# Performance work log

Measured on AMD Instinct MI355X. Metric: run time of the kernel, lower is better.

Reference implementation:

```python
import jax, jax.numpy as jnp
import numpy as np

B, S, H, NH = 2, 2048, 2048, 16
HD = H // NH  # head_dim = 128


def setup_inputs() -> dict:
    key = jax.random.key(0)
    ks = jax.random.split(key, 6)
    scale = 1.0 / np.sqrt(H)
    hidden_state = jax.random.normal(ks[0], (B, S, H), dtype=jnp.float32)
    # upper-triangular (strictly above diagonal) = 1 -> masked positions
    causal_mask = jnp.triu(jnp.ones((S, S), dtype=jnp.float32), k=1)[None, None]
    Wq = jax.random.normal(ks[1], (H, H), dtype=jnp.float32) * scale
    Wk = jax.random.normal(ks[2], (H, H), dtype=jnp.float32) * scale
    Wv = jax.random.normal(ks[3], (H, H), dtype=jnp.float32) * scale
    Wo = jax.random.normal(ks[4], (H, H), dtype=jnp.float32) * scale
    zeros = jnp.zeros((H,), dtype=jnp.float32)
    return {"hidden_state": hidden_state, "causal_mask": causal_mask,
            "Wq": Wq, "bq": zeros, "Wk": Wk, "bk": zeros,
            "Wv": Wv, "bv": zeros, "Wo": Wo, "bo": zeros}


def reference(hidden_state, causal_mask, Wq, bq, Wk, bk, Wv, bv, Wo, bo):
    b, s, h = hidden_state.shape
    q = (hidden_state @ Wq.T + bq).reshape(b, s, NH, HD).transpose(0, 2, 1, 3)  # [B,NH,S,HD]
    k = (hidden_state @ Wk.T + bk).reshape(b, s, NH, HD).transpose(0, 2, 1, 3)
    v = (hidden_state @ Wv.T + bv).reshape(b, s, NH, HD).transpose(0, 2, 1, 3)
    scores = jnp.einsum('bhqd,bhkd->bhqk', q, k) / jnp.sqrt(jnp.float32(HD))
    scores = scores + causal_mask * (-1e9)
    probs = jax.nn.softmax(scores, axis=-1)
    out = jnp.einsum('bhqk,bhkd->bhqd', probs, v)
    out = out.transpose(0, 2, 1, 3).reshape(b, s, h)
    return out @ Wo.T + bo
```

## Files before the change

kernel.cpp:

```cpp
#include <hip/hip_runtime.h>
#include <hip/hip_bf16.h>
#include <stdint.h>

#define B_   2
#define S_   2048
#define H_   2048
#define NH_  16
#define HD_  128
#define MTOT (B_*S_)

typedef __attribute__((ext_vector_type(8))) short bf16x8;
typedef __attribute__((ext_vector_type(4))) short bf16x4;
typedef __attribute__((ext_vector_type(4))) float f32x4;

__device__ __forceinline__ void gload_lds16(const void* g, void* l) {
    __builtin_amdgcn_global_load_lds(
        (const __attribute__((address_space(1))) void*)g,
        (__attribute__((address_space(3))) void*)l, 16, 0, 0);
}

__device__ __forceinline__ unsigned short f2bfu(float x) {
    __hip_bfloat16 h = __float2bfloat16(x);
    return *reinterpret_cast<unsigned short*>(&h);
}
__device__ __forceinline__ int packbf(float a, float b) {
    return (int)f2bfu(a) | ((int)f2bfu(b) << 16);
}

#define BAR()  asm volatile("s_barrier" ::: "memory")
#define WLG0() asm volatile("s_waitcnt lgkmcnt(0)" ::: "memory")
#define WVM(n) asm volatile("s_waitcnt vmcnt(" #n ")" ::: "memory")

__global__ void castall(const float* __restrict__ hs,
                        const float* __restrict__ w0, const float* __restrict__ w1,
                        const float* __restrict__ w2, const float* __restrict__ w3,
                        __hip_bfloat16* __restrict__ xb,
                        __hip_bfloat16* __restrict__ o0, __hip_bfloat16* __restrict__ o1,
                        __hip_bfloat16* __restrict__ o2, __hip_bfloat16* __restrict__ o3)
{
    const size_t Q = 1048576;
    const float* in; __hip_bfloat16* out; size_t base = 0;
    switch (blockIdx.y) {
        case 0:  in = hs; out = xb; break;
        case 1:  in = hs; out = xb; base = Q; break;
        case 2:  in = w0; out = o0; break;
        case 3:  in = w1; out = o1; break;
        case 4:  in = w2; out = o2; break;
        default: in = w3; out = o3; break;
    }
    size_t i = base + (size_t)blockIdx.x * 256 + threadIdx.x;
    float4 v = *(const float4*)(in + i * 4);
    uint2 o;
    o.x = (unsigned)packbf(v.x, v.y);
    o.y = (unsigned)packbf(v.z, v.w);
    *(uint2*)((char*)out + i * 8) = o;
}

template<int SMEMB, int BF16OUT>
__device__ __forceinline__ void gemm_body(const __hip_bfloat16* __restrict__ Ablk,
                                          const __hip_bfloat16* __restrict__ Wblk,
                                          const float* __restrict__ bias,
                                          void* __restrict__ Cout,
                                          int N, int K, int br, int bc)
{
    __shared__ __align__(16) char smem[SMEMB];
    __hip_bfloat16* As = (__hip_bfloat16*)smem;
    __hip_bfloat16* Bs = (__hip_bfloat16*)(smem + 8192);

    const int tid  = threadIdx.x;
    const int wave = tid >> 6, lane = tid & 63;
    const int quad = lane >> 4, l16 = lane & 15;
    const int wr = wave >> 1, wc = wave & 1;

    f32x4 acc[4][4] = {};

    for (int k0 = 0; k0 < K; k0 += 32) {
#pragma unroll
        for (int t = 0; t < 2; ++t) {
            int c = t * 256 + wave * 64 + lane;
            int row = c >> 2, cc = c & 3;
            int base = (t * 256 + wave * 64) * 16;
            gload_lds16(Ablk + (size_t)row * K + k0 + cc * 8, (char*)As + base);
            gload_lds16(Wblk + (size_t)row * K + k0 + cc * 8, (char*)Bs + base);
        }
        __syncthreads();

        bf16x8 af[4], bf[4];
#pragma unroll
        for (int i = 0; i < 4; ++i)
            af[i] = *(const bf16x8*)&As[(wr * 64 + i * 16 + l16) * 32 + quad * 8];
#pragma unroll
        for (int j = 0; j < 4; ++j)
            bf[j] = *(const bf16x8*)&Bs[(wc * 64 + j * 16 + l16) * 32 + quad * 8];

#pragma unroll
        for (int i = 0; i < 4; ++i)
#pragma unroll
            for (int j = 0; j < 4; ++j)
                acc[i][j] = __builtin_amdgcn_mfma_f32_16x16x32_bf16(af[i], bf[j], acc[i][j], 0, 0, 0);
        __syncthreads();
    }

#pragma unroll
    for (int i = 0; i < 4; ++i) {
        int row = br * 128 + wr * 64 + i * 16 + quad * 4;
#pragma unroll
        for (int j = 0; j < 4; ++j) {
            int col = bc * 128 + wc * 64 + j * 16 + l16;
            float bv = bias[col];
#pragma unroll
            for (int r = 0; r < 4; ++r) {
                float v = acc[i][j][r] + bv;
                if (BF16OUT)
                    ((__hip_bfloat16*)Cout)[(size_t)(row + r) * N + col] = __float2bfloat16(v);
                else
                    ((float*)Cout)[(size_t)(row + r) * N + col] = v;
            }
        }
    }
}

__global__ __launch_bounds__(256)
void gemm_out(const __hip_bfloat16* __restrict__ A, const __hip_bfloat16* __restrict__ W,
              const float* __restrict__ bias, float* __restrict__ C)
{
    gemm_body<16384, 0>(A + (size_t)(blockIdx.y * 128) * H_, W + (size_t)(blockIdx.x * 128) * H_,
                        bias, C, H_, H_, blockIdx.y, blockIdx.x);
}

template<int EPI>
__device__ __forceinline__ void gemm256x128_body(const __hip_bfloat16* __restrict__ Xp,
                                                 const __hip_bfloat16* __restrict__ Wp,
                                                 const float* __restrict__ bias,
                                                 void* __restrict__ Cout,
                                                 int bm, int bn, char* smem)
{
    const int tid  = threadIdx.x;
    const int wave = tid >> 6, lane = tid & 63;
    const int quad = lane >> 4, l16 = lane & 15;
    const int wr = wave >> 2, wc = wave & 3;

    const int ro = l16 * 64;
    const int co = (((l16 & 8) ? ((quad * 8) ^ 16) : (quad * 8)) << 1);

    int r0, c0, r1, c1;
    {
        int D = tid * 16;
        int rg = D >> 11, cg = (D >> 10) & 1;
        int rr = (D >> 6) & 15, c = (D & 63) >> 1;
        int cs = (rr & 8) ? (c ^ 16) : c;
        r0 = rg * 16 + rr;  c0 = cg * 32 + cs;
        D = 8192 + tid * 16;
        rg = D >> 11; cg = (D >> 10) & 1;
        rr = (D >> 6) & 15; c = (D & 63) >> 1;
        cs = (rr & 8) ? (c ^ 16) : c;
        r1 = rg * 16 + rr;  c1 = cg * 32 + cs;
    }

    char* const A0h = smem + wr * 16384;
    char* const A1h = smem + 32768 + wr * 16384;
    char* const B0h = smem + 65536 + (wc >> 1) * 8192;
    char* const B1h = smem + 81920 + (wc >> 1) * 8192;
    const int bsub = (wc & 1) * 2;

    auto STG = [&](char* ldsb, const __hip_bfloat16* g) {
        gload_lds16(g + (size_t)r0 * H_ + c0, ldsb + wave * 1024);
        gload_lds16(g + (size_t)r1 * H_ + c1, ldsb + 8192 + wave * 1024);
    };
    auto STG1 = [&](char* ldsb, const __hip_bfloat16* g) {
        gload_lds16(g + (size_t)r0 * H_ + c0, ldsb + wave * 1024);
    };
    auto SRCA = [&](const __hip_bfloat16* P, int t, int hf) {
        return P + (size_t)(hf * 128) * H_ + (size_t)t * 64;
    };
    auto SRCB = [&](const __hip_bfloat16* P, int t, int hf) {
        return P + (size_t)(hf * 64) * H_ + (size_t)t * 64;
    };

    f32x4 acc[8][2] = {};

    STG (smem,          SRCA(Xp, 0, 0));
    STG (smem + 16384,  SRCA(Xp, 0, 1));
    STG1(smem + 65536,        SRCB(Wp, 0, 0));
    STG1(smem + 65536 + 8192, SRCB(Wp, 0, 1));
    STG1(smem + 81920,        SRCB(Wp, 1, 0));
    STG1(smem + 81920 + 8192, SRCB(Wp, 1, 1));
    WVM(2);
    BAR();

    const int NIT = H_ / 128;
    bf16x8 bfr[2][2];
    for (int j = 0; j < NIT; ++j) {
        const bool more = (j < NIT - 1);
        const int t1 = 2 * j + 1;
#pragma unroll
        for (int ph = 0; ph < 8; ++ph) {
            const int p = ph & 3;
            char* aA = (ph < 4) ? A0h : A1h;
            char* aB = (ph < 4) ? B0h : B1h;

            if (p == 0) {
#pragma unroll
                for (int jj = 0; jj < 2; ++jj)
#pragma unroll
                    for (int kk = 0; kk < 2; ++kk)
                        bfr[jj][kk] = *(const bf16x8*)(aB + ((bsub + jj) * 2 + kk) * 1024 + ro + co);
            }
            bf16x8 af[2][2];
#pragma unroll
            for (int i2 = 0; i2 < 2; ++i2)
#pragma unroll
                for (int kk = 0; kk < 2; ++kk)
                    af[i2][kk] = *(const bf16x8*)(aA + ((2 * p + i2) * 2 + kk) * 1024 + ro + co);

            if (ph == 0) { STG(smem + 32768, SRCA(Xp, t1, 0));
                           STG(smem + 49152, SRCA(Xp, t1, 1)); }
            else if (ph == 1 && more) STG1(smem + 65536,        SRCB(Wp, t1 + 1, 0));
            else if (ph == 2 && more) STG1(smem + 65536 + 8192, SRCB(Wp, t1 + 1, 1));
            else if (ph == 4 && more) STG (smem,                SRCA(Xp, t1 + 1, 0));
            else if (ph == 5 && more) STG (smem + 16384,        SRCA(Xp, t1 + 1, 1));
            else if (ph == 6 && more) STG1(smem + 81920,        SRCB(Wp, t1 + 2, 0));
            else if (ph == 7 && more) STG1(smem + 81920 + 8192, SRCB(Wp, t1 + 2, 1));

            if (ph == 3) { if (more) { WVM(2); } else { WVM(0); } }
            if (ph == 7 && more) { WVM(2); }

            BAR();
            WLG0();
            __builtin_amdgcn_sched_barrier(0);
            __builtin_amdgcn_s_setprio(1);
#pragma unroll
            for (int kk = 0; kk < 2; ++kk)
#pragma unroll
                for (int i2 = 0; i2 < 2; ++i2)
#pragma unroll
                    for (int jj = 0; jj < 2; ++jj)
                        acc[2 * p + i2][jj] = __builtin_amdgcn_mfma_f32_16x16x32_bf16(
                            af[i2][kk], bfr[jj][kk], acc[2 * p + i2][jj], 0, 0, 0);
            __builtin_amdgcn_s_setprio(0);
            BAR();
        }
    }

    if (EPI == 2) {
        __hip_bfloat16* VTo = (__hip_bfloat16*)Cout;
#pragma unroll
        for (int i = 0; i < 8; ++i) {
            int tok = bm * 256 + wr * 128 + i * 16 + quad * 4;
            int b = tok >> 11, s = tok & (S_ - 1);
#pragma unroll
            for (int jj = 0; jj < 2; ++jj) {
                int col = bn * 128 + (wc >> 1) * 64 + (wc & 1) * 32 + jj * 16 + l16;
                int h = col >> 7, d = col & 127;
                float bv = bias[col];
                bf16x4 v;
#pragma unroll
                for (int r = 0; r < 4; ++r)
                    v[r] = (short)f2bfu(acc[i][jj][r] + bv);
                *(bf16x4*)(VTo + ((size_t)(b * 16 + h) * 128 + d) * S_ + s) = v;
            }
        }
    } else {
#pragma unroll
        for (int i = 0; i < 8; ++i) {
            int row = bm * 256 + wr * 128 + i * 16 + quad * 4;
#pragma unroll
            for (int jj = 0; jj < 2; ++jj) {
                int col = bn * 128 + (wc >> 1) * 64 + (wc & 1) * 32 + jj * 16 + l16;
                float bv = bias[col];
#pragma unroll
                for (int r = 0; r < 4; ++r)
                    ((__hip_bfloat16*)Cout)[(size_t)(row + r) * H_ + col] =
                        __float2bfloat16(acc[i][jj][r] + bv);
            }
        }
    }
}

__global__ __launch_bounds__(512, 2)
void gemm_qkv8(const __hip_bfloat16* __restrict__ X,
               const __hip_bfloat16* __restrict__ Wq, const __hip_bfloat16* __restrict__ Wk,
               const __hip_bfloat16* __restrict__ Wv,
               const float* __restrict__ bq, const float* __restrict__ bk,
               const float* __restrict__ bv,
               __hip_bfloat16* __restrict__ Qo, __hip_bfloat16* __restrict__ Ko,
               __hip_bfloat16* __restrict__ VTo)
{
    __shared__ __align__(16) char smem[98304];

    const int bid = blockIdx.x;
    const int swz = (bid & 7) * 96 + (bid >> 3);
    const int sel = swz >> 8;
    const int rem = swz & 255;
    const int bn  = rem & 15;
    const int bm  = rem >> 4;

    const __hip_bfloat16* W = (sel == 0) ? Wq : (sel == 1) ? Wk : Wv;
    const float* bias       = (sel == 0) ? bq : (sel == 1) ? bk : bv;

    const __hip_bfloat16* Xp = X + (size_t)(bm * 256) * H_;
    const __hip_bfloat16* Wp = W + (size_t)(bn * 128) * H_;

    if (sel == 2)
        gemm256x128_body<2>(Xp, Wp, bias, VTo, bm, bn, smem);
    else
        gemm256x128_body<1>(Xp, Wp, bias, (sel == 0) ? Qo : Ko, bm, bn, smem);
}

__global__ __launch_bounds__(256)
void attn_kernel(const __hip_bfloat16* __restrict__ Q,
                 const __hip_bfloat16* __restrict__ K,
                 const __hip_bfloat16* __restrict__ VT,
                 __hip_bfloat16* __restrict__ O)
{
    __shared__ __align__(16) char Ks[2][16384];
    __shared__ __align__(16) char Vt[2][16384];

    const int tid  = threadIdx.x;
    const int wave = tid >> 6, lane = tid & 63;
    const int quad = lane >> 4, l16 = lane & 15;

    const int lid = blockIdx.x;
    const int xcd = lid & 7;
    const int q   = lid >> 3;
    const int bh  = ((q >> 5) << 3) | xcd;
    const int qb  = 31 - (q & 31);
    const int b   = bh >> 4, h = bh & 15;

    const size_t headoff = (size_t)b * S_ * H_ + (size_t)h * HD_;
    const __hip_bfloat16* Qp  = Q + headoff;
    const __hip_bfloat16* Kp  = K + headoff;
    const __hip_bfloat16* Vtp = VT + (size_t)(b * 16 + h) * 128 * S_;

    const float scale  = 0.08838834764831843f;
    const float THRraw = 90.50966799187809f;
    const int A0 = (((quad & 1) * 2) * 16 + l16) * 4;
    const int A1 = A0 + 64;
    const bool hiq = (quad >= 2);

    const int qrow_local = wave * 16;
    const int qrow = qb * 64 + qrow_local;

    bf16x8 qf[4];
#pragma unroll
    for (int kd = 0; kd < 4; ++kd)
        qf[kd] = *(const bf16x8*)(Qp + (size_t)(qrow + l16) * H_ + kd * 32 + quad * 8);

    f32x4 oacc[8] = {};
    float mi = -1e30f, li = 0.0f;

#pragma unroll
    for (int t = 0; t < 4; ++t) {
        int c = wave * 256 + t * 64 + lane;
        int krow = c >> 4, kpos = c & 15;
        gload_lds16(Kp + (size_t)krow * H_ + (kpos ^ (krow & 7)) * 8,
                    &Ks[0][(wave * 256 + t * 64) * 16]);
        int vrow = c >> 3, vpos = c & 7;
        gload_lds16(Vtp + (size_t)vrow * S_ + (vpos ^ (vrow & 7)) * 8,
                    &Vt[0][(wave * 256 + t * 64) * 16]);
    }
    __syncthreads();

    for (int kb = 0; kb <= qb; ++kb) {
        const int cur = kb & 1;
        const bool more = (kb < qb);

        if (more) {
            const __hip_bfloat16* Kn = Kp + (size_t)(kb + 1) * 64 * H_;
            const int vcol = (kb + 1) * 64;
#pragma unroll
            for (int t = 0; t < 4; ++t) {
                int c = wave * 256 + t * 64 + lane;
                int krow = c >> 4, kpos = c & 15;
                gload_lds16(Kn + (size_t)krow * H_ + (kpos ^ (krow & 7)) * 8,
                            &Ks[cur ^ 1][(wave * 256 + t * 64) * 16]);
                int vrow = c >> 3, vpos = c & 7;
                gload_lds16(Vtp + (size_t)vrow * S_ + vcol + (vpos ^ (vrow & 7)) * 8,
                            &Vt[cur ^ 1][(wave * 256 + t * 64) * 16]);
            }
        }

        f32x4 sacc[4] = {};
#pragma unroll
        for (int cb = 0; cb < 4; ++cb) {
#pragma unroll
            for (int kd = 0; kd < 4; ++kd) {
                int row = cb * 16 + l16;
                int pos = (4 * kd + quad) ^ (l16 & 7);
                bf16x8 kf = *(const bf16x8*)&Ks[cur][row * 256 + pos * 16];
                sacc[cb] = __builtin_amdgcn_mfma_f32_16x16x32_bf16(kf, qf[kd], sacc[cb], 0, 0, 0);
            }
        }

        const bool diag = (kb == qb);
        float p[4][4];
        float tm = -1e30f;
#pragma unroll
        for (int cb = 0; cb < 4; ++cb)
#pragma unroll
            for (int r = 0; r < 4; ++r) {
                float s = sacc[cb][r];
                if (diag) {
                    int keyl = cb * 16 + quad * 4 + r;
                    if (keyl > qrow_local + l16) s = -1e30f;
                }
                p[cb][r] = s;
                tm = fmaxf(tm, s);
            }
        tm = fmaxf(tm, __shfl_xor(tm, 16));
        tm = fmaxf(tm, __shfl_xor(tm, 32));

        const bool noresc = __all(tm - mi <= THRraw);
        float mnew = noresc ? mi : fmaxf(mi, tm);
        float ms = mnew * scale;

        float sum = 0.0f;
#pragma unroll
        for (int cb = 0; cb < 4; ++cb)
#pragma unroll
            for (int r = 0; r < 4; ++r) {
                float e = __expf(__builtin_fmaf(p[cb][r], scale, -ms));
                p[cb][r] = e;
                sum += e;
            }
        sum += __shfl_xor(sum, 16);
        sum += __shfl_xor(sum, 32);

        if (noresc) {
            li = li + sum;
        } else {
            float alpha = __expf((mi - mnew) * scale);
            li = li * alpha + sum;
            float ar[4];
#pragma unroll
            for (int r = 0; r < 4; ++r)
                ar[r] = __shfl(alpha, quad * 4 + r);
#pragma unroll
            for (int db = 0; db < 8; ++db)
#pragma unroll
                for (int r = 0; r < 4; ++r)
                    oacc[db][r] *= ar[r];
        }
        mi = mnew;

        int Pp[4][2];
#pragma unroll
        for (int cb = 0; cb < 4; ++cb) {
            Pp[cb][0] = packbf(p[cb][0], p[cb][1]);
            Pp[cb][1] = packbf(p[cb][2], p[cb][3]);
        }
        bf16x8 pf[2];
#pragma unroll
        for (int ks = 0; ks < 2; ++ks) {
            int c0 = 2 * ks, c1 = 2 * ks + 1;
            int d0 = __builtin_amdgcn_ds_bpermute(A0, Pp[c0][0]);
            int e0 = __builtin_amdgcn_ds_bpermute(A0, Pp[c1][0]);
            int d1 = __builtin_amdgcn_ds_bpermute(A0, Pp[c0][1]);
            int e1 = __builtin_amdgcn_ds_bpermute(A0, Pp[c1][1]);
            int d2 = __builtin_amdgcn_ds_bpermute(A1, Pp[c0][0]);
            int e2 = __builtin_amdgcn_ds_bpermute(A1, Pp[c1][0]);
            int d3 = __builtin_amdgcn_ds_bpermute(A1, Pp[c0][1]);
            int e3 = __builtin_amdgcn_ds_bpermute(A1, Pp[c1][1]);
            union { int i[4]; bf16x8 v; } u;
            u.i[0] = hiq ? e0 : d0;
            u.i[1] = hiq ? e1 : d1;
            u.i[2] = hiq ? e2 : d2;
            u.i[3] = hiq ? e3 : d3;
            pf[ks] = u.v;
        }

#pragma unroll
        for (int ks = 0; ks < 2; ++ks) {
#pragma unroll
            for (int db = 0; db < 8; ++db) {
                int vrow = db * 16 + l16;
                int vpos = (ks * 4 + quad) ^ (l16 & 7);
                bf16x8 vf = *(const bf16x8*)&Vt[cur][vrow * 128 + vpos * 16];
                oacc[db] = __builtin_amdgcn_mfma_f32_16x16x32_bf16(pf[ks], vf, oacc[db], 0, 0, 0);
            }
        }

        __syncthreads();
    }

    float lr[4];
#pragma unroll
    for (int r = 0; r < 4; ++r)
        lr[r] = __shfl(li, quad * 4 + r);
#pragma unroll
    for (int db = 0; db < 8; ++db)
#pragma unroll
        for (int r = 0; r < 4; ++r) {
            float v = oacc[db][r] / lr[r];
            size_t row = (size_t)b * S_ + qrow + quad * 4 + r;
            O[row * H_ + h * HD_ + db * 16 + l16] = __float2bfloat16(v);
        }
}

extern "C" void kernel_launch(void* const* d_in, const int* in_sizes, int n_in,
                              void* d_out, int out_size, void* d_ws, size_t ws_size,
                              hipStream_t stream)
{
    const float* hs = (const float*)d_in[0];
    const float* Wq = (const float*)d_in[2];
    const float* bq = (const float*)d_in[3];
    const float* Wk = (const float*)d_in[4];
    const float* bk = (const float*)d_in[5];
    const float* Wv = (const float*)d_in[6];
    const float* bv = (const float*)d_in[7];
    const float* Wo = (const float*)d_in[8];
    const float* bo = (const float*)d_in[9];

    const size_t szX = (size_t)MTOT * H_;
    const size_t szW = (size_t)H_ * H_;

    __hip_bfloat16* Xbf = (__hip_bfloat16*)d_ws;
    __hip_bfloat16* Wqb = Xbf + szX;
    __hip_bfloat16* Wkb = Wqb + szW;
    __hip_bfloat16* Wvb = Wkb + szW;
    __hip_bfloat16* Wob = Wvb + szW;
    __hip_bfloat16* Qb  = Wob + szW;
    __hip_bfloat16* Kb  = Qb + szX;
    __hip_bfloat16* VTb = Kb + szX;

    castall<<<dim3(4096, 6), 256, 0, stream>>>(hs, Wq, Wk, Wv, Wo, Xbf, Wqb, Wkb, Wvb, Wob);

    gemm_qkv8<<<dim3(768), 512, 0, stream>>>(Xbf, Wqb, Wkb, Wvb, bq, bk, bv, Qb, Kb, VTb);

    attn_kernel<<<dim3(1024), 256, 0, stream>>>(Qb, Kb, VTb, Xbf);

    gemm_out<<<dim3(16, 32), 256, 0, stream>>>(Xbf, Wob, bo, (float*)d_out);
}
```

Measured before the change: 411.2 us.

## Process two adjacent query blocks per attention workgroup to reuse K/V tiles

Each attention workgroup now handles two consecutive 64-row query blocks (qbA, qbB) that share the same K/V tiles streamed into LDS, so each staged K and V fragment feeds two sets of MFMAs. The grid is halved to 512 blocks, with a reversed or forward ordering per group to balance causal work, and launch bounds request 2 blocks per CU. The cost being cut is LDS and global K/V traffic per unit of compute. In exchange, accumulator and Q register use doubles, which may reduce occupancy or cause spills, and the grid is smaller.

```diff
diff --git a/kernel.cpp b/kernel.cpp
--- a/kernel.cpp
+++ b/kernel.cpp
@@ -307,7 +307,7 @@
         gemm256x128_body<1>(Xp, Wp, bias, (sel == 0) ? Qo : Ko, bm, bn, smem);
 }
 
-__global__ __launch_bounds__(256)
+__global__ __launch_bounds__(256, 2)
 void attn_kernel(const __hip_bfloat16* __restrict__ Q,
                  const __hip_bfloat16* __restrict__ K,
                  const __hip_bfloat16* __restrict__ VT,
@@ -323,9 +323,12 @@
     const int lid = blockIdx.x;
     const int xcd = lid & 7;
     const int q   = lid >> 3;
-    const int bh  = ((q >> 5) << 3) | xcd;
-    const int qb  = 31 - (q & 31);
+    const int grp = q >> 4;
+    const int k15 = q & 15;
+    const int bh  = (grp << 3) | xcd;
+    const int u   = (grp < 2) ? (15 - k15) : k15;
     const int b   = bh >> 4, h = bh & 15;
+    const int qbA = 2 * u, qbB = 2 * u + 1;
 
     const size_t headoff = (size_t)b * S_ * H_ + (size_t)h * HD_;
     const __hip_bfloat16* Qp  = Q + headoff;
@@ -339,60 +342,22 @@
     const bool hiq = (quad >= 2);
 
     const int qrow_local = wave * 16;
-    const int qrow = qb * 64 + qrow_local;
-
-    bf16x8 qf[4];
-#pragma unroll
-    for (int kd = 0; kd < 4; ++kd)
-        qf[kd] = *(const bf16x8*)(Qp + (size_t)(qrow + l16) * H_ + kd * 32 + quad * 8);
-
-    f32x4 oacc[8] = {};
-    float mi = -1e30f, li = 0.0f;
-
-#pragma unroll
-    for (int t = 0; t < 4; ++t) {
-        int c = wave * 256 + t * 64 + lane;
-        int krow = c >> 4, kpos = c & 15;
-        gload_lds16(Kp + (size_t)krow * H_ + (kpos ^ (krow & 7)) * 8,
-                    &Ks[0][(wave * 256 + t * 64) * 16]);
-        int vrow = c >> 3, vpos = c & 7;
-        gload_lds16(Vtp + (size_t)vrow * S_ + (vpos ^ (vrow & 7)) * 8,
-                    &Vt[0][(wave * 256 + t * 64) * 16]);
-    }
-    __syncthreads();
-
-    for (int kb = 0; kb <= qb; ++kb) {
-        const int cur = kb & 1;
-        const bool more = (kb < qb);
-
-        if (more) {
-            const __hip_bfloat16* Kn = Kp + (size_t)(kb + 1) * 64 * H_;
-            const int vcol = (kb + 1) * 64;
-#pragma unroll
-            for (int t = 0; t < 4; ++t) {
-                int c = wave * 256 + t * 64 + lane;
-                int krow = c >> 4, kpos = c & 15;
-                gload_lds16(Kn + (size_t)krow * H_ + (kpos ^ (krow & 7)) * 8,
-                            &Ks[cur ^ 1][(wave * 256 + t * 64) * 16]);
-                int vrow = c >> 3, vpos = c & 7;
-                gload_lds16(Vtp + (size_t)vrow * S_ + vcol + (vpos ^ (vrow & 7)) * 8,
-                            &Vt[cur ^ 1][(wave * 256 + t * 64) * 16]);
-            }
-        }
-
-        f32x4 sacc[4] = {};
-#pragma unroll
-        for (int cb = 0; cb < 4; ++cb) {
-#pragma unroll
-            for (int kd = 0; kd < 4; ++kd) {
-                int row = cb * 16 + l16;
-                int pos = (4 * kd + quad) ^ (l16 & 7);
-                bf16x8 kf = *(const bf16x8*)&Ks[cur][row * 256 + pos * 16];
-                sacc[cb] = __builtin_amdgcn_mfma_f32_16x16x32_bf16(kf, qf[kd], sacc[cb], 0, 0, 0);
-            }
-        }
-
-        const bool diag = (kb == qb);
+    const int qrowA = qbA * 64 + qrow_local;
+    const int qrowB = qbB * 64 + qrow_local;
+
+    bf16x8 qfA[4], qfB[4];
+#pragma unroll
+    for (int kd = 0; kd < 4; ++kd) {
+        qfA[kd] = *(const bf16x8*)(Qp + (size_t)(qrowA + l16) * H_ + kd * 32 + quad * 8);
+        qfB[kd] = *(const bf16x8*)(Qp + (size_t)(qrowB + l16) * H_ + kd * 32 + quad * 8);
+    }
+
+    f32x4 oaccA[8] = {}, oaccB[8] = {};
+    float miA = -1e30f, liA = 0.0f;
+    float miB = -1e30f, liB = 0.0f;
+
+    auto sm_xform = [&](f32x4 (&sacc)[4], float& mi, float& li, f32x4 (&oacc)[8],
+                        bool diag, bf16x8 (&pf)[2]) {
         float p[4][4];
         float tm = -1e30f;
 #pragma unroll
@@ -449,7 +414,6 @@
             Pp[cb][0] = packbf(p[cb][0], p[cb][1]);
             Pp[cb][1] = packbf(p[cb][2], p[cb][3]);
         }
-        bf16x8 pf[2];
 #pragma unroll
         for (int ks = 0; ks < 2; ++ks) {
             int c0 = 2 * ks, c1 = 2 * ks + 1;
@@ -461,40 +425,118 @@
             int e2 = __builtin_amdgcn_ds_bpermute(A1, Pp[c1][0]);
             int d3 = __builtin_amdgcn_ds_bpermute(A1, Pp[c0][1]);
             int e3 = __builtin_amdgcn_ds_bpermute(A1, Pp[c1][1]);
-            union { int i[4]; bf16x8 v; } u;
-            u.i[0] = hiq ? e0 : d0;
-            u.i[1] = hiq ? e1 : d1;
-            u.i[2] = hiq ? e2 : d2;
-            u.i[3] = hiq ? e3 : d3;
-            pf[ks] = u.v;
-        }
-
-#pragma unroll
-        for (int ks = 0; ks < 2; ++ks) {
-#pragma unroll
-            for (int db = 0; db < 8; ++db) {
-                int vrow = db * 16 + l16;
-                int vpos = (ks * 4 + quad) ^ (l16 & 7);
-                bf16x8 vf = *(const bf16x8*)&Vt[cur][vrow * 128 + vpos * 16];
-                oacc[db] = __builtin_amdgcn_mfma_f32_16x16x32_bf16(pf[ks], vf, oacc[db], 0, 0, 0);
-            }
+            union { int i[4]; bf16x8 v; } w;
+            w.i[0] = hiq ? e0 : d0;
+            w.i[1] = hiq ? e1 : d1;
+            w.i[2] = hiq ? e2 : d2;
+            w.i[3] = hiq ? e3 : d3;
+            pf[ks] = w.v;
+        }
+    };
+
+#pragma unroll
+    for (int t = 0; t < 4; ++t) {
+        int c = wave * 256 + t * 64 + lane;
+        int krow = c >> 4, kpos = c & 15;
+        gload_lds16(Kp + (size_t)krow * H_ + (kpos ^ (krow & 7)) * 8,
+                    &Ks[0][(wave * 256 + t * 64) * 16]);
+        int vrow = c >> 3, vpos = c & 7;
+        gload_lds16(Vtp + (size_t)vrow * S_ + (vpos ^ (vrow & 7)) * 8,
+                    &Vt[0][(wave * 256 + t * 64) * 16]);
+    }
+    __syncthreads();
+
+    for (int kb = 0; kb <= qbB; ++kb) {
+        const int cur = kb & 1;
+        const bool more   = (kb < qbB);
+        const bool aliveA = (kb <= qbA);
+
+        if (more) {
+            const __hip_bfloat16* Kn = Kp + (size_t)(kb + 1) * 64 * H_;
+            const int vcol = (kb + 1) * 64;
+#pragma unroll
+            for (int t = 0; t < 4; ++t) {
+                int c = wave * 256 + t * 64 + lane;
+                int krow = c >> 4, kpos = c & 15;
+                gload_lds16(Kn + (size_t)krow * H_ + (kpos ^ (krow & 7)) * 8,
+                            &Ks[cur ^ 1][(wave * 256 + t * 64) * 16]);
+                int vrow = c >> 3, vpos = c & 7;
+                gload_lds16(Vtp + (size_t)vrow * S_ + vcol + (vpos ^ (vrow & 7)) * 8,
+                            &Vt[cur ^ 1][(wave * 256 + t * 64) * 16]);
+            }
+        }
+
+        f32x4 saccA[4] = {}, saccB[4] = {};
+#pragma unroll
+        for (int cb = 0; cb < 4; ++cb) {
+#pragma unroll
+            for (int kd = 0; kd < 4; ++kd) {
+                int row = cb * 16 + l16;
+                int pos = (4 * kd + quad) ^ (l16 & 7);
+                bf16x8 kf = *(const bf16x8*)&Ks[cur][row * 256 + pos * 16];
+                saccA[cb] = __builtin_amdgcn_mfma_f32_16x16x32_bf16(kf, qfA[kd], saccA[cb], 0, 0, 0);
+                saccB[cb] = __builtin_amdgcn_mfma_f32_16x16x32_bf16(kf, qfB[kd], saccB[cb], 0, 0, 0);
+            }
+        }
+
+        bf16x8 pfA[2], pfB[2];
+        if (aliveA) sm_xform(saccA, miA, liA, oaccA, kb == qbA, pfA);
+        sm_xform(saccB, miB, liB, oaccB, kb == qbB, pfB);
+
+        if (aliveA) {
+#pragma unroll
+            for (int ks = 0; ks < 2; ++ks)
+#pragma unroll
+                for (int db = 0; db < 8; ++db) {
+                    int vrow = db * 16 + l16;
+                    int vpos = (ks * 4 + quad) ^ (l16 & 7);
+                    bf16x8 vf = *(const bf16x8*)&Vt[cur][vrow * 128 + vpos * 16];
+                    oaccA[db] = __builtin_amdgcn_mfma_f32_16x16x32_bf16(pfA[ks], vf, oaccA[db], 0, 0, 0);
+                    oaccB[db] = __builtin_amdgcn_mfma_f32_16x16x32_bf16(pfB[ks], vf, oaccB[db], 0, 0, 0);
+                }
+        } else {
+#pragma unroll
+            for (int ks = 0; ks < 2; ++ks)
+#pragma unroll
+                for (int db = 0; db < 8; ++db) {
+                    int vrow = db * 16 + l16;
+                    int vpos = (ks * 4 + quad) ^ (l16 & 7);
+                    bf16x8 vf = *(const bf16x8*)&Vt[cur][vrow * 128 + vpos * 16];
+                    oaccB[db] = __builtin_amdgcn_mfma_f32_16x16x32_bf16(pfB[ks], vf, oaccB[db], 0, 0, 0);
+                }
         }
 
         __syncthreads();
     }
 
-    float lr[4];
-#pragma unroll
-    for (int r = 0; r < 4; ++r)
-        lr[r] = __shfl(li, quad * 4 + r);
-#pragma unroll
-    for (int db = 0; db < 8; ++db)
-#pragma unroll
-        for (int r = 0; r < 4; ++r) {
-            float v = oacc[db][r] / lr[r];
-            size_t row = (size_t)b * S_ + qrow + quad * 4 + r;
-            O[row * H_ + h * HD_ + db * 16 + l16] = __float2bfloat16(v);
-        }
+    {
+        float lr[4];
+#pragma unroll
+        for (int r = 0; r < 4; ++r)
+            lr[r] = __shfl(liA, quad * 4 + r);
+#pragma unroll
+        for (int db = 0; db < 8; ++db)
+#pragma unroll
+            for (int r = 0; r < 4; ++r) {
+                float v = oaccA[db][r] / lr[r];
+                size_t row = (size_t)b * S_ + qrowA + quad * 4 + r;
+                O[row * H_ + h * HD_ + db * 16 + l16] = __float2bfloat16(v);
+            }
+    }
+    {
+        float lr[4];
+#pragma unroll
+        for (int r = 0; r < 4; ++r)
+            lr[r] = __shfl(liB, quad * 4 + r);
+#pragma unroll
+        for (int db = 0; db < 8; ++db)
+#pragma unroll
+            for (int r = 0; r < 4; ++r) {
+                float v = oaccB[db][r] / lr[r];
+                size_t row = (size_t)b * S_ + qrowB + quad * 4 + r;
+                O[row * H_ + h * HD_ + db * 16 + l16] = __float2bfloat16(v);
+            }
+    }
 }
 
 extern "C" void kernel_launch(void* const* d_in, const int* in_sizes, int n_in,
@@ -527,7 +569,7 @@
 
     gemm_qkv8<<<dim3(768), 512, 0, stream>>>(Xbf, Wqb, Wkb, Wvb, bq, bk, bv, Qb, Kb, VTb);
 
-    attn_kernel<<<dim3(1024), 256, 0, stream>>>(Qb, Kb, VTb, Xbf);
+    attn_kernel<<<dim3(512), 256, 0, stream>>>(Qb, Kb, VTb, Xbf);
 
     gemm_out<<<dim3(16, 32), 256, 0, stream>>>(Xbf, Wob, bo, (float*)d_out);
 }
```

Result: faster. 390.7 us (-5.0%).
